# Kernel tuning notes

Hardware: AMD Instinct MI355X
Metric: run time of the kernel (lower is better)

## Reference

```python
import jax, jax.numpy as jnp
import numpy as np

N, F, H, R, DEG, K = 8192, 64, 128, 3, 32, 32
TEMP = 0.3          # config.edge_temperature
NEG_SLOPE = 0.2     # LeakyReLU slope
EPS_LN = 1e-5
W_THRESH = 1e-6


def setup_inputs() -> dict:
    key = jax.random.key(0)
    ks = jax.random.split(key, 16)
    E = N * DEG
    # each node has DEG outgoing edges so no softmax row is empty (-inf everywhere)
    src = jnp.repeat(jnp.arange(N), DEG)
    tgt = jax.random.randint(ks[0], (E,), 0, N)
    edge_index = jnp.stack([src, tgt]).astype(jnp.int64)
    x = jax.random.normal(ks[1], (N, F), jnp.float32)
    edge_attr = jax.random.normal(ks[2], (E, 3), jnp.float32)
    s = lambda k, sh: jax.random.normal(k, sh, jnp.float32) * 0.05
    D = 2 * F + 3  # edge_input_dim
    params = dict(
        Ws1=s(ks[3], (D, H)), bs1=jnp.zeros(H), ln_g=jnp.ones(H), ln_b=jnp.zeros(H),
        Ws2=s(ks[4], (H, 1)), bs2=jnp.zeros(1),
        Wp=s(ks[5], (D, H)), bp=jnp.zeros(H),
        Wr1=s(ks[6], (F, H)), br1=jnp.zeros(H), Wr2=s(ks[7], (H, R)), br2=jnp.zeros(R),
        Wg1=s(ks[8], (R, H, H // 2)), bg1=jnp.zeros((R, H // 2)),
        Wg2=s(ks[9], (R, H // 2, 1)), bg2=jnp.zeros((R, 1)),
        Wc1=s(ks[10], (F, H)), bc1=jnp.zeros(H), Wc2=s(ks[11], (H, 1)), bc2=jnp.zeros(1),
    )
    return {"x": x, "edge_index": edge_index, "edge_attr": edge_attr, **params}


def reference(x, edge_index, edge_attr,
              Ws1, bs1, ln_g, ln_b, Ws2, bs2, Wp, bp,
              Wr1, br1, Wr2, br2, Wg1, bg1, Wg2, bg2,
              Wc1, bc1, Wc2, bc2):
    src, tgt = edge_index[0], edge_index[1]
    num_nodes = x.shape[0]

    # regime encoder on global mean state
    gs = x.mean(axis=0)
    regime_probs = jax.nn.softmax(jax.nn.relu(gs @ Wr1 + br1) @ Wr2 + br2)  # [R]

    # contagion detector (scalar level)
    contagion_level = jax.nn.sigmoid(jax.nn.relu(x @ Wc1 + bc1) @ Wc2 + bc2).mean()

    # gather -> edge MLP scorer with LayerNorm + LeakyReLU
    edge_input = jnp.concatenate([x[src], x[tgt], edge_attr], axis=-1)  # [E, 2F+3]
    h = edge_input @ Ws1 + bs1
    mu = h.mean(-1, keepdims=True)
    var = h.var(-1, keepdims=True)
    h = (h - mu) * jax.lax.rsqrt(var + EPS_LN) * ln_g + ln_b
    h = jnp.where(h >= 0, h, NEG_SLOPE * h)
    edge_scores_raw = h @ Ws2 + bs2  # [E, 1]

    # regime gating
    edge_hidden = jax.nn.relu(edge_input @ Wp + bp)  # [E, H]
    g1 = jax.nn.relu(jnp.einsum('eh,rhm->erm', edge_hidden, Wg1) + bg1)
    gates = jax.nn.sigmoid(jnp.einsum('erm,rmo->ero', g1, Wg2) + bg2)[..., 0]  # [E, R]
    gate_combined = (gates * regime_probs).sum(-1, keepdims=True)  # [E, 1]

    amp = 1.0 + 0.5 * contagion_level
    edge_scores = (edge_scores_raw * gate_combined * amp)[:, 0]  # [E]

    # scatter into dense NxN, masked softmax per source row, top-k
    M = jnp.full((num_nodes, num_nodes), -jnp.inf, x.dtype).at[src, tgt].set(edge_scores)
    P = jax.nn.softmax(M / TEMP, axis=-1)  # [N, N]
    topk_values, topk_indices = jax.lax.top_k(P, K)  # [N, K]

    # in-device compaction equivalent: weights below threshold zeroed (dropped edges)
    new_edge_weights = jnp.where(topk_values > W_THRESH, topk_values, 0.0)  # [N, K]
    return new_edge_weights, topk_indices
```

## Files before the change

kernel.cpp:

```cpp
#include <hip/hip_runtime.h>
#include <hip/hip_bf16.h>
#include <math.h>

#define NN 8192
#define FF 64
#define HH 128
#define RR 3
#define DEG 32
#define KK 32
#define EE (NN*DEG)
#define DD 131
#define TEMP 0.3f
#define NEG_SLOPE 0.2f
#define EPS_LN 1e-5f
#define W_THRESH 1e-6f

typedef float v2f __attribute__((ext_vector_type(2)));
__device__ __forceinline__ float4 ld4(const float* p) { return *(const float4*)p; }
#define PKFMA(a, b, c) __builtin_elementwise_fma((a), (b), (c))
#define AIDX(a, j) a[((j)>>2)*2 + (((j)&3)>>1)][(j)&1]
#define GIDX(r, g) gaccv[r][(g)>>1][(g)&1]


__global__ __launch_bounds__(256) void stats_kernel(
    const float* __restrict__ x, const float* __restrict__ Wc1,
    const float* __restrict__ bc1, const float* __restrict__ Wc2,
    const float* __restrict__ bc2, float* __restrict__ hdr)
{
    __shared__ float xs[64 * 65];
    __shared__ float wl[64 * 128];
    __shared__ float cs[4][64];
    int t = threadIdx.x;
    int n0 = blockIdx.x * 64;

    for (int i = 0; i < 16; i++) {
        int flat = t + i * 256;
        int r = flat >> 6, c = flat & 63;
        xs[r * 65 + c] = x[(n0 + r) * 64 + c];
    }
    for (int i = 0; i < 32; i++) {
        int flat = t + i * 256;
        wl[flat] = Wc1[flat];
    }
    __syncthreads();

    {
        int col = t & 63, g = t >> 6;
        float ps = 0.f;
        for (int r = g * 16; r < g * 16 + 16; r++) ps += xs[r * 65 + col];
        cs[g][col] = ps;
    }
    __syncthreads();
    if (t < 64) {
        float v = cs[0][t] + cs[1][t] + cs[2][t] + cs[3][t];
        atomicAdd(&hdr[8 + t], v);
    }

    int r = t >> 2, q = t & 3;
    float accl = 0.f;
    for (int hh = 0; hh < 32; hh++) {
        int h = hh * 4 + q;
        float s = bc1[h];
        for (int i = 0; i < 64; i++) s += xs[r * 65 + i] * wl[i * 128 + h];
        accl += fmaxf(s, 0.f) * Wc2[h];
    }
    accl += __shfl_xor(accl, 1);
    accl += __shfl_xor(accl, 2);
    if (q == 0) {
        float lvl = 1.f / (1.f + expf(-(accl + bc2[0])));
        atomicAdd(&hdr[0], lvl);
    }
}

__global__ __launch_bounds__(128) void regime_kernel(
    const float* __restrict__ Wr1, const float* __restrict__ br1,
    const float* __restrict__ Wr2, const float* __restrict__ br2,
    float* __restrict__ hdr)
{
    __shared__ float gsl[64];
    __shared__ float t1[128];
    int t = threadIdx.x;
    if (t < 64) gsl[t] = hdr[8 + t] * (1.f / (float)NN);
    __syncthreads();
    float a = br1[t];
    for (int i = 0; i < 64; i++) a += gsl[i] * Wr1[i * 128 + t];
    t1[t] = fmaxf(a, 0.f);
    __syncthreads();
    if (t < 3) {
        float v = br2[t];
        for (int h = 0; h < 128; h++) v += t1[h] * Wr2[h * 3 + t];
        gsl[32 + t] = v;
    }
    __syncthreads();
    if (t == 0) {
        float v0 = gsl[32], v1 = gsl[33], v2 = gsl[34];
        float m = fmaxf(v0, fmaxf(v1, v2));
        float e0 = expf(v0 - m), e1 = expf(v1 - m), e2 = expf(v2 - m);
        float inv = 1.f / (e0 + e1 + e2);
        hdr[1] = e0 * inv; hdr[2] = e1 * inv; hdr[3] = e2 * inv;
        hdr[4] = 1.f + 0.5f * (hdr[0] * (1.f / (float)NN));
    }
}

__global__ __launch_bounds__(256) void partial_kernel(
    const float* __restrict__ x, const float* __restrict__ Ws1,
    const float* __restrict__ Wp, float* __restrict__ PA)
{
    __shared__ float xs[32 * 65];
    __shared__ float wl[64 * 128];
    int t = threadIdx.x;
    int which = blockIdx.x & 1;
    int n0 = (blockIdx.x >> 1) * 32;
    const float* base = which ? Wp : Ws1;

    for (int i = t; i < 2048; i += 256)
        xs[(i >> 6) * 65 + (i & 63)] = x[n0 * 64 + i];
    for (int it = 0; it < 8; it++) {
        int flat = (t + it * 256) * 4;
        *(float4*)&wl[flat] = ld4(&base[flat]);
    }
    __syncthreads();

    int row = t >> 3, colg = t & 7;
    float acc[16];
    #pragma unroll
    for (int j = 0; j < 16; j++) acc[j] = 0.f;
    const float* xr = &xs[row * 65];
    for (int k = 0; k < 64; k++) {
        float a = xr[k];
        const float* wr = &wl[k * 128 + colg * 16];
        #pragma unroll
        for (int jj = 0; jj < 4; jj++) {
            float4 w = ld4(wr + 4 * jj);
            acc[4*jj+0] += a * w.x; acc[4*jj+1] += a * w.y;
            acc[4*jj+2] += a * w.z; acc[4*jj+3] += a * w.w;
        }
    }
    float* outp = PA + (size_t)which * (NN * 128) + (size_t)(n0 + row) * 128 + colg * 16;
    #pragma unroll
    for (int j = 0; j < 16; j++) outp[j] = acc[j];
}

#define EIB_S 76
__global__ __launch_bounds__(256) void edge_fused_kernel(
    const int* __restrict__ tgt_idx, const float* __restrict__ edge_attr,
    const float* __restrict__ x,
    const float* __restrict__ Ws1, const float* __restrict__ bs1,
    const float* __restrict__ ln_g, const float* __restrict__ ln_b,
    const float* __restrict__ Ws2, const float* __restrict__ bs2,
    const float* __restrict__ Wp, const float* __restrict__ bp,
    const float* __restrict__ Wg1, const float* __restrict__ bg1,
    const float* __restrict__ Wg2, const float* __restrict__ bg2,
    const float* __restrict__ PA1, const float* __restrict__ PA2,
    const float* __restrict__ hdr, float* __restrict__ scores)
{
    __shared__ float pool[8000];
    float* EIB   = pool;
    float* WPan  = pool + 4864;
    float* ehTh  = pool;
    float* WgPan = pool + 4352;
    float* Gbuf  = pool;
    float* rawS  = pool + 7936;

    int t = threadIdx.x;
    int e0 = blockIdx.x * 64;

    {
        int r = t >> 2, q = t & 3;
        int ge = e0 + r;
        int tg = tgt_idx[ge];
        #pragma unroll
        for (int i = 0; i < 4; i++) {
            int col = q * 16 + 4 * i;
            *(float4*)&EIB[r * EIB_S + col] = ld4(&x[tg * 64 + col]);
        }
        if (q == 0) {
            float4 v;
            v.x = edge_attr[(size_t)ge * 3 + 0];
            v.y = edge_attr[(size_t)ge * 3 + 1];
            v.z = edge_attr[(size_t)ge * 3 + 2];
            v.w = 0.f;
            *(float4*)&EIB[r * EIB_S + 64] = v;
        } else if (q == 1) {
            *(float4*)&EIB[r * EIB_S + 68] = make_float4(0.f, 0.f, 0.f, 0.f);
        } else if (q == 2) {
            *(float4*)&EIB[r * EIB_S + 72] = make_float4(0.f, 0.f, 0.f, 0.f);
        }
    }

    int tcol = t & 7, trow = t >> 3;
    const float* EIr0 = &EIB[(2 * trow) * EIB_S];
    const float* EIr1 = EIr0 + EIB_S;
    int src = (e0 + 2 * trow) >> 5;

    v2f accs0[8], accs1[8], accp0[8], accp1[8];

    {
        const float* p1 = &PA1[(size_t)src * 128 + tcol * 4];
        const float* p2 = &PA2[(size_t)src * 128 + tcol * 4];
        #pragma unroll
        for (int jj = 0; jj < 4; jj++) {
            float4 v;
            v = ld4(p1 + jj * 32);
            v2f lo1 = { v.x, v.y }, hi1 = { v.z, v.w };
            accs0[jj*2] = lo1; accs0[jj*2+1] = hi1;
            accs1[jj*2] = lo1; accs1[jj*2+1] = hi1;
            v = ld4(p2 + jj * 32);
            v2f lo2 = { v.x, v.y }, hi2 = { v.z, v.w };
            accp0[jj*2] = lo2; accp0[jj*2+1] = hi2;
            accp1[jj*2] = lo2; accp1[jj*2+1] = hi2;
        }
    }

    for (int p = 0; p < 6; p++) {
        __syncthreads();
        #pragma unroll
        for (int i = 0; i < 3; i++) {
            int fid = i * 256 + t;
            int mat = (fid >= 384) ? 1 : 0;
            int loc = fid - mat * 384;
            int pr = loc >> 5;
            int pc = (loc & 31) * 4;
            int wrow = 64 + p * 12 + pr;
            const float* Wsrc = mat ? Wp : Ws1;
            float4 w = (wrow < 131) ? ld4(&Wsrc[wrow * 128 + pc])
                                    : make_float4(0.f, 0.f, 0.f, 0.f);
            *(float4*)&WPan[mat * 1536 + pr * 128 + pc] = w;
        }
        __syncthreads();
        for (int kk = 0; kk < 12; kk++) {
            int k = p * 12 + kk;
            float a0 = EIr0[k];
            float a1 = EIr1[k];
            v2f a0v = { a0, a0 }, a1v = { a1, a1 };
            const float* ws = &WPan[kk * 128 + tcol * 4];
            const float* wq = ws + 1536;
            #pragma unroll
            for (int jj = 0; jj < 4; jj++) {
                float4 w1 = ld4(ws + jj * 32);
                v2f w1a = { w1.x, w1.y }, w1b = { w1.z, w1.w };
                accs0[jj*2]   = PKFMA(a0v, w1a, accs0[jj*2]);
                accs0[jj*2+1] = PKFMA(a0v, w1b, accs0[jj*2+1]);
                accs1[jj*2]   = PKFMA(a1v, w1a, accs1[jj*2]);
                accs1[jj*2+1] = PKFMA(a1v, w1b, accs1[jj*2+1]);
                float4 w2 = ld4(wq + jj * 32);
                v2f w2a = { w2.x, w2.y }, w2b = { w2.z, w2.w };
                accp0[jj*2]   = PKFMA(a0v, w2a, accp0[jj*2]);
                accp0[jj*2+1] = PKFMA(a0v, w2b, accp0[jj*2+1]);
                accp1[jj*2]   = PKFMA(a1v, w2a, accp1[jj*2]);
                accp1[jj*2+1] = PKFMA(a1v, w2b, accp1[jj*2+1]);
            }
        }
    }

    {
        float s0 = 0.f, ss0 = 0.f, s1 = 0.f, ss1 = 0.f;
        #pragma unroll
        for (int j = 0; j < 16; j++) {
            int col = tcol * 4 + (j >> 2) * 32 + (j & 3);
            float b = bs1[col];
            float u0 = AIDX(accs0, j) + b;  AIDX(accs0, j) = u0;
            float u1 = AIDX(accs1, j) + b;  AIDX(accs1, j) = u1;
            s0 += u0; ss0 += u0 * u0;
            s1 += u1; ss1 += u1 * u1;
        }
        #pragma unroll
        for (int m = 1; m < 8; m <<= 1) {
            s0 += __shfl_xor(s0, m);  ss0 += __shfl_xor(ss0, m);
            s1 += __shfl_xor(s1, m);  ss1 += __shfl_xor(ss1, m);
        }
        float mu0 = s0 * (1.f / 128.f), mu1 = s1 * (1.f / 128.f);
        float var0 = ss0 * (1.f / 128.f) - mu0 * mu0;
        float var1 = ss1 * (1.f / 128.f) - mu1 * mu1;
        float inv0 = 1.f / sqrtf(var0 + EPS_LN);
        float inv1 = 1.f / sqrtf(var1 + EPS_LN);
        float d0 = 0.f, d1 = 0.f;
        #pragma unroll
        for (int j = 0; j < 16; j++) {
            int col = tcol * 4 + (j >> 2) * 32 + (j & 3);
            float g = ln_g[col], bb = ln_b[col], w2 = Ws2[col];
            float y0 = (AIDX(accs0, j) - mu0) * inv0 * g + bb;
            float y1 = (AIDX(accs1, j) - mu1) * inv1 * g + bb;
            y0 = (y0 >= 0.f) ? y0 : NEG_SLOPE * y0;
            y1 = (y1 >= 0.f) ? y1 : NEG_SLOPE * y1;
            d0 += y0 * w2; d1 += y1 * w2;
        }
        #pragma unroll
        for (int m = 1; m < 8; m <<= 1) {
            d0 += __shfl_xor(d0, m); d1 += __shfl_xor(d1, m);
        }
        if (tcol == 0) {
            rawS[2 * trow]     = d0 + bs2[0];
            rawS[2 * trow + 1] = d1 + bs2[0];
        }
    }

    int gtr = t >> 4, gtc = t & 15;
    int grow = t >> 2, gq = t & 3;

    v2f gaccv[3][8];
    #pragma unroll
    for (int rr = 0; rr < 3; rr++)
        #pragma unroll
        for (int j = 0; j < 8; j++) gaccv[rr][j] = (v2f){ 0.f, 0.f };

    for (int hf = 0; hf < 2; hf++) {
        __syncthreads();
        #pragma unroll
        for (int j2 = 0; j2 < 8; j2++) {
            int j = hf * 8 + j2;
            int col = tcol * 4 + (j >> 2) * 32 + (j & 3);
            int lc = col - hf * 64;
            float b = bp[col];
            ehTh[lc * 68 + 2 * trow]     = fmaxf(AIDX(accp0, j) + b, 0.f);
            ehTh[lc * 68 + 2 * trow + 1] = fmaxf(AIDX(accp1, j) + b, 0.f);
        }
        for (int p = 0; p < 4; p++) {
            __syncthreads();
            #pragma unroll
            for (int i = 0; i < 3; i++) {
                int fid = i * 256 + t;
                int rr = fid >> 8;
                int loc = fid & 255;
                int pr = loc >> 4;
                int pc = (loc & 15) * 4;
                *(float4*)&WgPan[rr * 1024 + pr * 64 + pc] =
                    ld4(&Wg1[(size_t)(rr * 128 + hf * 64 + p * 16 + pr) * 64 + pc]);
            }
            __syncthreads();
            for (int kk = 0; kk < 16; kk++) {
                float4 av = ld4(&ehTh[(p * 16 + kk) * 68 + 4 * gtr]);
                v2f ax = { av.x, av.x }, ay = { av.y, av.y };
                v2f az = { av.z, av.z }, aw = { av.w, av.w };
                #pragma unroll
                for (int rr = 0; rr < 3; rr++) {
                    float4 bv = ld4(&WgPan[rr * 1024 + kk * 64 + 4 * gtc]);
                    v2f bva = { bv.x, bv.y }, bvb = { bv.z, bv.w };
                    gaccv[rr][0] = PKFMA(ax, bva, gaccv[rr][0]);
                    gaccv[rr][1] = PKFMA(ax, bvb, gaccv[rr][1]);
                    gaccv[rr][2] = PKFMA(ay, bva, gaccv[rr][2]);
                    gaccv[rr][3] = PKFMA(ay, bvb, gaccv[rr][3]);
                    gaccv[rr][4] = PKFMA(az, bva, gaccv[rr][4]);
                    gaccv[rr][5] = PKFMA(az, bvb, gaccv[rr][5]);
                    gaccv[rr][6] = PKFMA(aw, bva, gaccv[rr][6]);
                    gaccv[rr][7] = PKFMA(aw, bvb, gaccv[rr][7]);
                }
            }
        }
    }

    float gc = 0.f;
    for (int rr = 0; rr < 3; rr++) {
        __syncthreads();
        #pragma unroll
        for (int j = 0; j < 4; j++) {
            float b = bg1[rr * 64 + 4 * gtc + j];
            float4 g;
            g.x = fmaxf(GIDX(rr, 0  + j) + b, 0.f);
            g.y = fmaxf(GIDX(rr, 4  + j) + b, 0.f);
            g.z = fmaxf(GIDX(rr, 8  + j) + b, 0.f);
            g.w = fmaxf(GIDX(rr, 12 + j) + b, 0.f);
            *(float4*)&Gbuf[(4 * gtc + j) * 68 + 4 * gtr] = g;
        }
        __syncthreads();
        float pacc = 0.f;
        #pragma unroll
        for (int j = 0; j < 16; j++) {
            int m = gq * 4 + (j >> 2) * 16 + (j & 3);
            pacc += Gbuf[m * 68 + grow] * Wg2[rr * 64 + m];
        }
        pacc += __shfl_xor(pacc, 1);
        pacc += __shfl_xor(pacc, 2);
        float gate = 1.f / (1.f + expf(-(pacc + bg2[rr])));
        gc += gate * hdr[1 + rr];
    }
    if (gq == 0) scores[e0 + grow] = rawS[grow] * gc * hdr[4];
}

__global__ __launch_bounds__(64) void finalize_kernel(
    const int* __restrict__ tgt_idx, const float* __restrict__ scores,
    float* __restrict__ out_w, float* __restrict__ out_i)
{
    __shared__ int   tl[32];
    __shared__ float pl[32];
    int j = threadIdx.x;
    int row = blockIdx.x;
    bool lane_active = (j < 32);
    int   tg = 0;
    float s  = -INFINITY;
    if (lane_active) {
        tg = tgt_idx[row * 32 + j];
        s  = scores[row * 32 + j];
        tl[j] = tg;
    }
    __syncthreads();

    bool alive = false;
    if (lane_active) {
        alive = true;
        for (int j2 = j + 1; j2 < 32; j2++)
            if (tl[j2] == tg) { alive = false; break; }
    }
    float z = (lane_active && alive) ? s * (1.f / TEMP) : -INFINITY;
    float m = z;
    #pragma unroll
    for (int mm = 1; mm < 64; mm <<= 1) m = fmaxf(m, __shfl_xor(m, mm));
    float p = (lane_active && alive) ? expf(z - m) : 0.f;
    float sum = p;
    #pragma unroll
    for (int mm = 1; mm < 64; mm <<= 1) sum += __shfl_xor(sum, mm);
    p = p / sum;
    if (lane_active) pl[j] = alive ? p : -1.f;
    __syncthreads();

    int rank = 0, dcount = 0;
    for (int j2 = 0; j2 < 32; j2++) {
        float pj = pl[j2];
        if (pj >= 0.f) {
            dcount++;
            if (lane_active && alive) {
                if (pj > p || (pj == p && tl[j2] < tg)) rank++;
            }
        }
    }
    if (lane_active && alive) {
        out_w[row * 32 + rank] = (p > W_THRESH) ? p : 0.f;
        out_i[row * 32 + rank] = (float)tg;
    }
    if (j == 0) {
        int c = 0;
        for (int slot = dcount; slot < 32; slot++) {
            for (;;) {
                bool found = false;
                for (int q = 0; q < 32; q++) if (tl[q] == c) { found = true; break; }
                if (!found) break;
                c++;
            }
            out_w[row * 32 + slot] = 0.f;
            out_i[row * 32 + slot] = (float)c;
            c++;
        }
    }
}

extern "C" void kernel_launch(void* const* d_in, const int* in_sizes, int n_in,
                              void* d_out, int out_size, void* d_ws, size_t ws_size,
                              hipStream_t stream)
{
    const float* x          = (const float*)d_in[0];
    const int*   edge_index = (const int*)  d_in[1];
    const float* edge_attr  = (const float*)d_in[2];
    const float* Ws1 = (const float*)d_in[3];
    const float* bs1 = (const float*)d_in[4];
    const float* ln_g = (const float*)d_in[5];
    const float* ln_b = (const float*)d_in[6];
    const float* Ws2 = (const float*)d_in[7];
    const float* bs2 = (const float*)d_in[8];
    const float* Wp  = (const float*)d_in[9];
    const float* bp  = (const float*)d_in[10];
    const float* Wr1 = (const float*)d_in[11];
    const float* br1 = (const float*)d_in[12];
    const float* Wr2 = (const float*)d_in[13];
    const float* br2 = (const float*)d_in[14];
    const float* Wg1 = (const float*)d_in[15];
    const float* bg1 = (const float*)d_in[16];
    const float* Wg2 = (const float*)d_in[17];
    const float* bg2 = (const float*)d_in[18];
    const float* Wc1 = (const float*)d_in[19];
    const float* bc1 = (const float*)d_in[20];
    const float* Wc2 = (const float*)d_in[21];
    const float* bc2 = (const float*)d_in[22];

    float* hdr    = (float*)d_ws;
    float* scores = hdr + 128;
    float* tabs   = scores + EE;
    const int* tgt = edge_index + EE;

    hipMemsetAsync(d_ws, 0, 512, stream);
    stats_kernel<<<128, 256, 0, stream>>>(x, Wc1, bc1, Wc2, bc2, hdr);
    regime_kernel<<<1, 128, 0, stream>>>(Wr1, br1, Wr2, br2, hdr);
    partial_kernel<<<(NN / 32) * 2, 256, 0, stream>>>(x, Ws1, Wp, tabs);
    edge_fused_kernel<<<EE / 64, 256, 0, stream>>>(
        tgt, edge_attr, x, Ws1, bs1, ln_g, ln_b, Ws2, bs2, Wp, bp,
        Wg1, bg1, Wg2, bg2, tabs, tabs + (size_t)NN * 128, hdr, scores);
    finalize_kernel<<<NN, 64, 0, stream>>>(
        tgt, scores, (float*)d_out, (float*)d_out + NN * KK);
}
```

Measured before the change: 455.8 us.

## Fuse finalize softmax/top-k into edge kernel and double edges per block

The per-row softmax, dedup and ranking stage is folded into the end of the edge MLP kernel. This removes the separate finalize launch and the global round trip of the scores array. The edge kernel now handles 128 edges (4 source rows) per 512-thread block, so each staged weight panel is reused across twice as many edges, and the activation reads in the first GEMM are vectorized to float4. In exchange, LDS use per block grows and the 512-thread launch bound may force register spills or lower occupancy.

```diff
diff --git a/kernel.cpp b/kernel.cpp
--- a/kernel.cpp
+++ b/kernel.cpp
@@ -142,7 +142,8 @@
 }
 
 #define EIB_S 76
-__global__ __launch_bounds__(256) void edge_fused_kernel(
+#define EHT_S 132
+__global__ __launch_bounds__(512) void edge_fused_kernel(
     const int* __restrict__ tgt_idx, const float* __restrict__ edge_attr,
     const float* __restrict__ x,
     const float* __restrict__ Ws1, const float* __restrict__ bs1,
@@ -152,18 +153,22 @@
     const float* __restrict__ Wg1, const float* __restrict__ bg1,
     const float* __restrict__ Wg2, const float* __restrict__ bg2,
     const float* __restrict__ PA1, const float* __restrict__ PA2,
-    const float* __restrict__ hdr, float* __restrict__ scores)
+    const float* __restrict__ hdr,
+    float* __restrict__ out_w, float* __restrict__ out_i)
 {
-    __shared__ float pool[8000];
+    __shared__ float pool[12928];
+    __shared__ int   tlS[4][33];
+    __shared__ float plS[4][33];
+    __shared__ float scrS[128];
     float* EIB   = pool;
-    float* WPan  = pool + 4864;
+    float* WPan  = pool + 9728;
     float* ehTh  = pool;
-    float* WgPan = pool + 4352;
+    float* WgPan = pool + 8448;
     float* Gbuf  = pool;
-    float* rawS  = pool + 7936;
+    float* rawS  = pool + 12800;
 
     int t = threadIdx.x;
-    int e0 = blockIdx.x * 64;
+    int e0 = blockIdx.x * 128;
 
     {
         int r = t >> 2, q = t & 3;
@@ -215,40 +220,47 @@
     for (int p = 0; p < 6; p++) {
         __syncthreads();
         #pragma unroll
-        for (int i = 0; i < 3; i++) {
-            int fid = i * 256 + t;
-            int mat = (fid >= 384) ? 1 : 0;
-            int loc = fid - mat * 384;
-            int pr = loc >> 5;
-            int pc = (loc & 31) * 4;
-            int wrow = 64 + p * 12 + pr;
-            const float* Wsrc = mat ? Wp : Ws1;
-            float4 w = (wrow < 131) ? ld4(&Wsrc[wrow * 128 + pc])
-                                    : make_float4(0.f, 0.f, 0.f, 0.f);
-            *(float4*)&WPan[mat * 1536 + pr * 128 + pc] = w;
-        }
-        __syncthreads();
-        for (int kk = 0; kk < 12; kk++) {
-            int k = p * 12 + kk;
-            float a0 = EIr0[k];
-            float a1 = EIr1[k];
-            v2f a0v = { a0, a0 }, a1v = { a1, a1 };
-            const float* ws = &WPan[kk * 128 + tcol * 4];
-            const float* wq = ws + 1536;
+        for (int i = 0; i < 2; i++) {
+            int fid = i * 512 + t;
+            if (fid < 768) {
+                int mat = (fid >= 384) ? 1 : 0;
+                int loc = fid - mat * 384;
+                int pr = loc >> 5;
+                int pc = (loc & 31) * 4;
+                int wrow = 64 + p * 12 + pr;
+                const float* Wsrc = mat ? Wp : Ws1;
+                float4 w = (wrow < 131) ? ld4(&Wsrc[wrow * 128 + pc])
+                                        : make_float4(0.f, 0.f, 0.f, 0.f);
+                *(float4*)&WPan[mat * 1536 + pr * 128 + pc] = w;
+            }
+        }
+        __syncthreads();
+        for (int kk0 = 0; kk0 < 12; kk0 += 4) {
+            float4 a04 = ld4(EIr0 + p * 12 + kk0);
+            float4 a14 = ld4(EIr1 + p * 12 + kk0);
+            float a0s[4] = { a04.x, a04.y, a04.z, a04.w };
+            float a1s[4] = { a14.x, a14.y, a14.z, a14.w };
             #pragma unroll
-            for (int jj = 0; jj < 4; jj++) {
-                float4 w1 = ld4(ws + jj * 32);
-                v2f w1a = { w1.x, w1.y }, w1b = { w1.z, w1.w };
-                accs0[jj*2]   = PKFMA(a0v, w1a, accs0[jj*2]);
-                accs0[jj*2+1] = PKFMA(a0v, w1b, accs0[jj*2+1]);
-                accs1[jj*2]   = PKFMA(a1v, w1a, accs1[jj*2]);
-                accs1[jj*2+1] = PKFMA(a1v, w1b, accs1[jj*2+1]);
-                float4 w2 = ld4(wq + jj * 32);
-                v2f w2a = { w2.x, w2.y }, w2b = { w2.z, w2.w };
-                accp0[jj*2]   = PKFMA(a0v, w2a, accp0[jj*2]);
-                accp0[jj*2+1] = PKFMA(a0v, w2b, accp0[jj*2+1]);
-                accp1[jj*2]   = PKFMA(a1v, w2a, accp1[jj*2]);
-                accp1[jj*2+1] = PKFMA(a1v, w2b, accp1[jj*2+1]);
+            for (int u = 0; u < 4; u++) {
+                int kk = kk0 + u;
+                v2f a0v = { a0s[u], a0s[u] }, a1v = { a1s[u], a1s[u] };
+                const float* ws = &WPan[kk * 128 + tcol * 4];
+                const float* wq = ws + 1536;
+                #pragma unroll
+                for (int jj = 0; jj < 4; jj++) {
+                    float4 w1 = ld4(ws + jj * 32);
+                    v2f w1a = { w1.x, w1.y }, w1b = { w1.z, w1.w };
+                    accs0[jj*2]   = PKFMA(a0v, w1a, accs0[jj*2]);
+                    accs0[jj*2+1] = PKFMA(a0v, w1b, accs0[jj*2+1]);
+                    accs1[jj*2]   = PKFMA(a1v, w1a, accs1[jj*2]);
+                    accs1[jj*2+1] = PKFMA(a1v, w1b, accs1[jj*2+1]);
+                    float4 w2 = ld4(wq + jj * 32);
+                    v2f w2a = { w2.x, w2.y }, w2b = { w2.z, w2.w };
+                    accp0[jj*2]   = PKFMA(a0v, w2a, accp0[jj*2]);
+                    accp0[jj*2+1] = PKFMA(a0v, w2b, accp0[jj*2+1]);
+                    accp1[jj*2]   = PKFMA(a1v, w2a, accp1[jj*2]);
+                    accp1[jj*2+1] = PKFMA(a1v, w2b, accp1[jj*2+1]);
+                }
             }
         }
     }
@@ -312,24 +324,26 @@
             int col = tcol * 4 + (j >> 2) * 32 + (j & 3);
             int lc = col - hf * 64;
             float b = bp[col];
-            ehTh[lc * 68 + 2 * trow]     = fmaxf(AIDX(accp0, j) + b, 0.f);
-            ehTh[lc * 68 + 2 * trow + 1] = fmaxf(AIDX(accp1, j) + b, 0.f);
+            ehTh[lc * EHT_S + 2 * trow]     = fmaxf(AIDX(accp0, j) + b, 0.f);
+            ehTh[lc * EHT_S + 2 * trow + 1] = fmaxf(AIDX(accp1, j) + b, 0.f);
         }
         for (int p = 0; p < 4; p++) {
             __syncthreads();
             #pragma unroll
-            for (int i = 0; i < 3; i++) {
-                int fid = i * 256 + t;
-                int rr = fid >> 8;
-                int loc = fid & 255;
-                int pr = loc >> 4;
-                int pc = (loc & 15) * 4;
-                *(float4*)&WgPan[rr * 1024 + pr * 64 + pc] =
-                    ld4(&Wg1[(size_t)(rr * 128 + hf * 64 + p * 16 + pr) * 64 + pc]);
+            for (int i = 0; i < 2; i++) {
+                int fid = i * 512 + t;
+                if (fid < 768) {
+                    int rr = fid >> 8;
+                    int loc = fid & 255;
+                    int pr = loc >> 4;
+                    int pc = (loc & 15) * 4;
+                    *(float4*)&WgPan[rr * 1024 + pr * 64 + pc] =
+                        ld4(&Wg1[(size_t)(rr * 128 + hf * 64 + p * 16 + pr) * 64 + pc]);
+                }
             }
             __syncthreads();
             for (int kk = 0; kk < 16; kk++) {
-                float4 av = ld4(&ehTh[(p * 16 + kk) * 68 + 4 * gtr]);
+                float4 av = ld4(&ehTh[(p * 16 + kk) * EHT_S + 4 * gtr]);
                 v2f ax = { av.x, av.x }, ay = { av.y, av.y };
                 v2f az = { av.z, av.z }, aw = { av.w, av.w };
                 #pragma unroll
@@ -360,85 +374,82 @@
             g.y = fmaxf(GIDX(rr, 4  + j) + b, 0.f);
             g.z = fmaxf(GIDX(rr, 8  + j) + b, 0.f);
             g.w = fmaxf(GIDX(rr, 12 + j) + b, 0.f);
-            *(float4*)&Gbuf[(4 * gtc + j) * 68 + 4 * gtr] = g;
+            *(float4*)&Gbuf[(4 * gtc + j) * EHT_S + 4 * gtr] = g;
         }
         __syncthreads();
         float pacc = 0.f;
         #pragma unroll
         for (int j = 0; j < 16; j++) {
             int m = gq * 4 + (j >> 2) * 16 + (j & 3);
-            pacc += Gbuf[m * 68 + grow] * Wg2[rr * 64 + m];
+            pacc += Gbuf[m * EHT_S + grow] * Wg2[rr * 64 + m];
         }
         pacc += __shfl_xor(pacc, 1);
         pacc += __shfl_xor(pacc, 2);
         float gate = 1.f / (1.f + expf(-(pacc + bg2[rr])));
         gc += gate * hdr[1 + rr];
     }
-    if (gq == 0) scores[e0 + grow] = rawS[grow] * gc * hdr[4];
-}
-
-__global__ __launch_bounds__(64) void finalize_kernel(
-    const int* __restrict__ tgt_idx, const float* __restrict__ scores,
-    float* __restrict__ out_w, float* __restrict__ out_i)
-{
-    __shared__ int   tl[32];
-    __shared__ float pl[32];
-    int j = threadIdx.x;
-    int row = blockIdx.x;
-    bool lane_active = (j < 32);
-    int   tg = 0;
-    float s  = -INFINITY;
-    if (lane_active) {
-        tg = tgt_idx[row * 32 + j];
-        s  = scores[row * 32 + j];
-        tl[j] = tg;
-    }
-    __syncthreads();
-
-    bool alive = false;
-    if (lane_active) {
-        alive = true;
-        for (int j2 = j + 1; j2 < 32; j2++)
-            if (tl[j2] == tg) { alive = false; break; }
-    }
-    float z = (lane_active && alive) ? s * (1.f / TEMP) : -INFINITY;
-    float m = z;
-    #pragma unroll
-    for (int mm = 1; mm < 64; mm <<= 1) m = fmaxf(m, __shfl_xor(m, mm));
-    float p = (lane_active && alive) ? expf(z - m) : 0.f;
-    float sum = p;
-    #pragma unroll
-    for (int mm = 1; mm < 64; mm <<= 1) sum += __shfl_xor(sum, mm);
-    p = p / sum;
-    if (lane_active) pl[j] = alive ? p : -1.f;
-    __syncthreads();
-
-    int rank = 0, dcount = 0;
-    for (int j2 = 0; j2 < 32; j2++) {
-        float pj = pl[j2];
-        if (pj >= 0.f) {
-            dcount++;
-            if (lane_active && alive) {
-                if (pj > p || (pj == p && tl[j2] < tg)) rank++;
-            }
-        }
-    }
-    if (lane_active && alive) {
-        out_w[row * 32 + rank] = (p > W_THRESH) ? p : 0.f;
-        out_i[row * 32 + rank] = (float)tg;
-    }
-    if (j == 0) {
-        int c = 0;
-        for (int slot = dcount; slot < 32; slot++) {
-            for (;;) {
-                bool found = false;
-                for (int q = 0; q < 32; q++) if (tl[q] == c) { found = true; break; }
-                if (!found) break;
-                c++;
-            }
-            out_w[row * 32 + slot] = 0.f;
-            out_i[row * 32 + slot] = (float)c;
-            c++;
+    if (gq == 0) scrS[grow] = rawS[grow] * gc * hdr[4];
+
+    __syncthreads();
+    {
+        int rowl = t >> 6, j = t & 63;
+        bool act = (t < 256) && (j < 32);
+        int tg = 0;
+        float s = -INFINITY;
+        if (act) {
+            tg = tgt_idx[e0 + rowl * 32 + j];
+            s = scrS[rowl * 32 + j];
+            tlS[rowl][j] = tg;
+        }
+        __syncthreads();
+        bool alive = false;
+        if (act) {
+            alive = true;
+            for (int j2 = j + 1; j2 < 32; j2++)
+                if (tlS[rowl][j2] == tg) { alive = false; break; }
+        }
+        float z = (act && alive) ? s * (1.f / TEMP) : -INFINITY;
+        float m = z;
+        #pragma unroll
+        for (int mm = 1; mm < 64; mm <<= 1) m = fmaxf(m, __shfl_xor(m, mm));
+        float p = (act && alive) ? expf(z - m) : 0.f;
+        float sum = p;
+        #pragma unroll
+        for (int mm = 1; mm < 64; mm <<= 1) sum += __shfl_xor(sum, mm);
+        p = p / sum;
+        if (act) plS[rowl][j] = alive ? p : -1.f;
+        __syncthreads();
+
+        if (t < 256) {
+            int row = blockIdx.x * 4 + rowl;
+            int rank = 0, dcount = 0;
+            for (int j2 = 0; j2 < 32; j2++) {
+                float pj = plS[rowl][j2];
+                if (pj >= 0.f) {
+                    dcount++;
+                    if (act && alive) {
+                        if (pj > p || (pj == p && tlS[rowl][j2] < tg)) rank++;
+                    }
+                }
+            }
+            if (act && alive) {
+                out_w[row * 32 + rank] = (p > W_THRESH) ? p : 0.f;
+                out_i[row * 32 + rank] = (float)tg;
+            }
+            if (j == 0) {
+                int c = 0;
+                for (int slot = dcount; slot < 32; slot++) {
+                    for (;;) {
+                        bool found = false;
+                        for (int q = 0; q < 32; q++) if (tlS[rowl][q] == c) { found = true; break; }
+                        if (!found) break;
+                        c++;
+                    }
+                    out_w[row * 32 + slot] = 0.f;
+                    out_i[row * 32 + slot] = (float)c;
+                    c++;
+                }
+            }
         }
     }
 }
@@ -471,18 +482,16 @@
     const float* Wc2 = (const float*)d_in[21];
     const float* bc2 = (const float*)d_in[22];
 
-    float* hdr    = (float*)d_ws;
-    float* scores = hdr + 128;
-    float* tabs   = scores + EE;
+    float* hdr  = (float*)d_ws;
+    float* tabs = hdr + 128;
     const int* tgt = edge_index + EE;
 
     hipMemsetAsync(d_ws, 0, 512, stream);
     stats_kernel<<<128, 256, 0, stream>>>(x, Wc1, bc1, Wc2, bc2, hdr);
     regime_kernel<<<1, 128, 0, stream>>>(Wr1, br1, Wr2, br2, hdr);
     partial_kernel<<<(NN / 32) * 2, 256, 0, stream>>>(x, Ws1, Wp, tabs);
-    edge_fused_kernel<<<EE / 64, 256, 0, stream>>>(
+    edge_fused_kernel<<<EE / 128, 512, 0, stream>>>(
         tgt, edge_attr, x, Ws1, bs1, ln_g, ln_b, Ws2, bs2, Wp, bp,
-        Wg1, bg1, Wg2, bg2, tabs, tabs + (size_t)NN * 128, hdr, scores);
-    finalize_kernel<<<NN, 64, 0, stream>>>(
-        tgt, scores, (float*)d_out, (float*)d_out + NN * KK);
+        Wg1, bg1, Wg2, bg2, tabs, tabs + (size_t)NN * 128, hdr,
+        (float*)d_out, (float*)d_out + NN * KK);
 }
```

Result: slower. 517.2 us (+13.5%).
